# Kernel tuning notes

Measured on AMD Instinct MI355X. Metric: run time of the kernel, lower is better.

The kernel has to match this reference:

```python
import jax, jax.numpy as jnp
import numpy as np

BN_EPS = 1e-5


def setup_inputs() -> dict:
    key = jax.random.key(0)
    ks = jax.random.split(key, 12)
    B, C, S, M = 128, 512, 128, 512  # batch, model_dim, spatial_size, middle_ss
    lim_in = 1.0 / np.sqrt(S)   # torch Linear init bound, fan_in = S
    lim_mid = 1.0 / np.sqrt(M)
    return {
        "query": jax.random.normal(ks[0], (B, C, S), jnp.float32),
        "key":   jax.random.normal(ks[1], (B, C, S), jnp.float32),
        "value": jax.random.normal(ks[2], (B, C, S), jnp.float32),
        "Wq": jax.random.uniform(ks[3], (M, S), jnp.float32, -lim_in, lim_in),
        "bq": jax.random.uniform(ks[4], (M,), jnp.float32, -lim_in, lim_in),
        "Wk": jax.random.uniform(ks[5], (M, S), jnp.float32, -lim_in, lim_in),
        "bk": jax.random.uniform(ks[6], (M,), jnp.float32, -lim_in, lim_in),
        "Wv": jax.random.uniform(ks[7], (M, S), jnp.float32, -lim_in, lim_in),
        "bv": jax.random.uniform(ks[8], (M,), jnp.float32, -lim_in, lim_in),
        "Wf": jax.random.uniform(ks[9], (S, M), jnp.float32, -lim_mid, lim_mid),
        "bf": jax.random.uniform(ks[10], (S,), jnp.float32, -lim_mid, lim_mid),
        "gamma": jnp.ones((C,), jnp.float32),
        "beta": jnp.zeros((C,), jnp.float32),
    }


def reference(query, key, value, Wq, bq, Wk, bk, Wv, bv, Wf, bf, gamma, beta):
    residual = value                                  # [B, C, S]
    q = jnp.einsum('bcs,ms->bcm', query, Wq) + bq     # [B, C, M]
    k = jnp.einsum('bcs,ms->bcm', key, Wk) + bk
    v = jnp.einsum('bcs,ms->bcm', value, Wv) + bv
    scale = k.shape[-1] ** (-0.5)
    scores = jnp.einsum('bim,bjm->bij', q, k) * scale  # [B, C, C]
    attention = jax.nn.softmax(scores, axis=2)
    context = jnp.einsum('bij,bjm->bim', attention, v)  # [B, C, M]
    out = jnp.einsum('bcm,sm->bcs', context, Wf) + bf    # [B, C, S]
    # BatchNorm1d (training mode): stats over (batch, spatial) per channel
    mean = jnp.mean(out, axis=(0, 2), keepdims=True)
    var = jnp.mean(jnp.square(out - mean), axis=(0, 2), keepdims=True)
    out = (out - mean) * jax.lax.rsqrt(var + BN_EPS)
    out = out * gamma[None, :, None] + beta[None, :, None]
    out = jax.nn.relu(out)
    out = residual + out
    return (out, attention)
```

## Files before the change

kernel.cpp:

```cpp
#include <hip/hip_runtime.h>
#include <math.h>

#define B_  128
#define C_  512
#define S_  128
#define M_  512
#define BN_EPS 1e-5f

typedef __attribute__((ext_vector_type(8))) short   short8;
typedef __attribute__((ext_vector_type(4))) float   floatx4;
typedef __attribute__((ext_vector_type(4))) unsigned short ushort4v;
typedef __attribute__((ext_vector_type(8))) unsigned short ushort8v;

__device__ __forceinline__ unsigned short f2bu(float f) {
    union { float f; unsigned int u; } c; c.f = f;
    unsigned int u = c.u;
    return (unsigned short)((u + 0x7fffu + ((u >> 16) & 1u)) >> 16);
}

__global__ __launch_bounds__(256)
void f2bf4_kernel(const float* __restrict__ a0, const float* __restrict__ a1,
                  const float* __restrict__ a2, const float* __restrict__ a3,
                  unsigned short* __restrict__ out, long n8)
{
    const float* in = (blockIdx.y == 0) ? a0 : (blockIdx.y == 1) ? a1
                    : (blockIdx.y == 2) ? a2 : a3;
    unsigned short* o = out + (long)blockIdx.y * (n8 * 8);
    const long i = (long)blockIdx.x * 256 + threadIdx.x;
    if (i >= n8) return;
    const float4* p = (const float4*)in + 2 * i;
    const float4 x = p[0], y = p[1];
    ushort4v u0, u1;
    u0.x = f2bu(x.x); u0.y = f2bu(x.y); u0.z = f2bu(x.z); u0.w = f2bu(x.w);
    u1.x = f2bu(y.x); u1.y = f2bu(y.y); u1.z = f2bu(y.z); u1.w = f2bu(y.w);
    ((ushort4v*)o)[2 * i]     = u0;
    ((ushort4v*)o)[2 * i + 1] = u1;
}

__global__ __launch_bounds__(256)
void pack_bias_zero_stats(const float* __restrict__ bq, const float* __restrict__ bk,
                          const float* __restrict__ bv, float* __restrict__ bqkv,
                          float* __restrict__ stats)
{
    const int t = blockIdx.x * 256 + threadIdx.x;
    if (t < 512)            bqkv[t] = bq[t];
    else if (t < 1024)      bqkv[t] = bk[t - 512];
    else if (t < 1536)      bqkv[t] = bv[t - 1024];
    else if (t < 1536 + 2 * C_) stats[t - 1536] = 0.f;
}

__global__ __launch_bounds__(512, 4)
void proj_kernel(const float* __restrict__ qf, const float* __restrict__ kf,
                 const float* __restrict__ vf, const unsigned short* __restrict__ Wbf,
                 const float* __restrict__ bqkv, unsigned short* __restrict__ outbf)
{
    const int z = blockIdx.y;
    const float* A = (z == 0 ? qf : z == 1 ? kf : vf) + (long)blockIdx.x * 64 * S_;
    const unsigned short* W = Wbf + (long)z * M_ * S_;
    const float* bias = bqkv + z * M_;
    unsigned short* O = outbf + (long)z * ((long)B_ * C_ * M_) + (long)blockIdx.x * 64 * M_;

    __shared__ unsigned short As[64][40];
    __shared__ unsigned short Bs[512][40];

    const int t    = threadIdx.x;
    const int lane = t & 63;
    const int wave = t >> 6;
    const int lrow = lane & 15;
    const int quad = lane >> 4;
    const int cb   = wave * 64;

    floatx4 acc[4][4] = {};

    const int ar = t >> 3;
    const int ac = (t & 7) * 4;
    const int sr = t >> 2;
    const int sc = (t & 3) * 8;

    for (int k0 = 0; k0 < S_; k0 += 32) {
        const float4 av = *(const float4*)(A + (long)ar * S_ + k0 + ac);
        ushort4v au;
        au.x = f2bu(av.x); au.y = f2bu(av.y); au.z = f2bu(av.z); au.w = f2bu(av.w);
        *(ushort4v*)&As[ar][ac] = au;
        #pragma unroll
        for (int i = 0; i < 4; ++i) {
            const int r = sr + i * 128;
            *(short8*)&Bs[r][sc] = *(const short8*)(W + (long)r * S_ + k0 + sc);
        }
        __syncthreads();

        short8 af[4];
        #pragma unroll
        for (int i = 0; i < 4; ++i)
            af[i] = *(const short8*)&As[i * 16 + lrow][quad * 8];
        #pragma unroll
        for (int j = 0; j < 4; ++j) {
            const short8 bfr = *(const short8*)&Bs[cb + j * 16 + lrow][quad * 8];
            #pragma unroll
            for (int i = 0; i < 4; ++i)
                acc[i][j] = __builtin_amdgcn_mfma_f32_16x16x32_bf16(
                    af[i], bfr, acc[i][j], 0, 0, 0);
        }
        __syncthreads();
    }

    unsigned short* scr = &Bs[wave * 64][0];
    const int rr = lane >> 3;
    const int rc = (lane & 7) * 8;
    #pragma unroll
    for (int i = 0; i < 4; ++i) {
        #pragma unroll
        for (int j = 0; j < 4; ++j) {
            const float bv = bias[cb + j * 16 + lrow];
            #pragma unroll
            for (int rg = 0; rg < 4; ++rg)
                scr[(quad * 4 + rg) * 72 + j * 16 + lrow] = f2bu(acc[i][j][rg] + bv);
        }
        #pragma unroll
        for (int p = 0; p < 2; ++p) {
            const int row = p * 8 + rr;
            const ushort8v v = *(const ushort8v*)&scr[row * 72 + rc];
            *(ushort8v*)&O[(long)(i * 16 + row) * M_ + cb + rc] = v;
        }
    }
}

template<bool STATS>
__global__ __launch_bounds__(256)
void gemm_bf16(const unsigned short* __restrict__ A, const unsigned short* __restrict__ Bm,
               const float* __restrict__ bias, void* __restrict__ Cc,
               int M, int N, int K, int ldA, int ldB, int ldC,
               long sA, long sB, long sC, long sBias, float scale, int outMode,
               float* __restrict__ statsOut)
{
    const int bz = blockIdx.z;
    A  += (long)bz * sA;
    Bm += (long)bz * sB;
    if (bias) bias += (long)bz * sBias;

    __shared__ unsigned short As[128][72];
    __shared__ unsigned short Bs[128][72];

    const int t    = threadIdx.x;
    const int lane = t & 63;
    const int wave = t >> 6;
    const int wm   = (wave >> 1) * 64;
    const int wn   = (wave & 1) * 64;
    const int lrow = lane & 15;
    const int quad = lane >> 4;
    const int row0 = blockIdx.x * 128;
    const int col0 = blockIdx.y * 128;

    floatx4 acc[4][4] = {};

    const int srow = t >> 3;
    const int skc  = (t & 7) * 8;

    for (int k0 = 0; k0 < K; k0 += 64) {
        #pragma unroll
        for (int i = 0; i < 4; ++i) {
            const int r = srow + i * 32;
            *(short8*)&As[r][skc] =
                *(const short8*)(A + (long)(row0 + r) * ldA + k0 + skc);
            *(short8*)&Bs[r][skc] =
                *(const short8*)(Bm + (long)(col0 + r) * ldB + k0 + skc);
        }
        __syncthreads();

        #pragma unroll
        for (int kb = 0; kb < 2; ++kb) {
            short8 af[4], bfr[4];
            #pragma unroll
            for (int i = 0; i < 4; ++i)
                af[i]  = *(const short8*)&As[wm + i * 16 + lrow][kb * 32 + quad * 8];
            #pragma unroll
            for (int j = 0; j < 4; ++j)
                bfr[j] = *(const short8*)&Bs[wn + j * 16 + lrow][kb * 32 + quad * 8];
            #pragma unroll
            for (int i = 0; i < 4; ++i)
                #pragma unroll
                for (int j = 0; j < 4; ++j)
                    acc[i][j] = __builtin_amdgcn_mfma_f32_16x16x32_bf16(
                        af[i], bfr[j], acc[i][j], 0, 0, 0);
        }
        __syncthreads();
    }

    float rs[4][4], rss[4][4];
    if (STATS) {
        #pragma unroll
        for (int i = 0; i < 4; ++i)
            #pragma unroll
            for (int rg = 0; rg < 4; ++rg) { rs[i][rg] = 0.f; rss[i][rg] = 0.f; }
    }
    #pragma unroll
    for (int j = 0; j < 4; ++j) {
        const int col = col0 + wn + j * 16 + lrow;
        const float bv = bias ? bias[col] : 0.0f;
        #pragma unroll
        for (int i = 0; i < 4; ++i) {
            const int rbase = row0 + wm + i * 16 + quad * 4;
            #pragma unroll
            for (int reg = 0; reg < 4; ++reg) {
                const float val = acc[i][j][reg] * scale + bv;
                const int r = rbase + reg;
                if (STATS) { rs[i][reg] += val; rss[i][reg] += val * val; }
                if (outMode == 0) {
                    ((float*)Cc)[(long)bz * sC + (long)r * ldC + col] = val;
                } else if (outMode == 1) {
                    ((unsigned short*)Cc)[(long)bz * sC + (long)r * ldC + col] = f2bu(val);
                } else {
                    ((unsigned short*)Cc)[((long)(r >> 9)) * 65536 + (long)col * 512 + (r & 511)] = f2bu(val);
                }
            }
        }
    }
    if (STATS) {
        #pragma unroll
        for (int i = 0; i < 4; ++i) {
            #pragma unroll
            for (int reg = 0; reg < 4; ++reg) {
                float s = rs[i][reg], ss = rss[i][reg];
                #pragma unroll
                for (int off = 1; off < 16; off <<= 1) {
                    s  += __shfl_xor(s,  off);
                    ss += __shfl_xor(ss, off);
                }
                if (lrow == 0) {
                    const int r = row0 + wm + i * 16 + quad * 4 + reg;
                    atomicAdd(&statsOut[r],      s);
                    atomicAdd(&statsOut[C_ + r], ss);
                }
            }
        }
    }
}

__global__ __launch_bounds__(512, 4)
void scores_softmax_kernel(const unsigned short* __restrict__ q_bf,
                           const unsigned short* __restrict__ k_bf,
                           float* __restrict__ attn,
                           unsigned short* __restrict__ attnbf,
                           float scale)
{
    const int bid = blockIdx.x;
    const int b   = (bid & 7) * 16 + ((bid >> 3) >> 3);
    const int r0  = ((bid >> 3) & 7) * 64;

    const unsigned short* qg = q_bf + (long)b * C_ * M_;
    const unsigned short* kg = k_bf + (long)b * C_ * M_;
    float* ab           = attn   + (long)b * C_ * C_;
    unsigned short* abf = attnbf + (long)b * C_ * C_;

    __shared__ unsigned short qs[64][40];
    __shared__ unsigned short ks[512][40];
    __shared__ float red[64][9];

    const int t    = threadIdx.x;
    const int lane = t & 63;
    const int wave = t >> 6;
    const int lrow = lane & 15;
    const int quad = lane >> 4;
    const int cb   = wave * 64;

    floatx4 acc[4][4] = {};

    const int sr = t >> 2;
    const int sc = (t & 3) * 8;

    for (int k0 = 0; k0 < M_; k0 += 32) {
        if (t < 256)
            *(short8*)&qs[t >> 2][sc] =
                *(const short8*)(qg + (long)(r0 + (t >> 2)) * M_ + k0 + sc);
        #pragma unroll
        for (int i = 0; i < 4; ++i) {
            const int r = sr + i * 128;
            *(short8*)&ks[r][sc] = *(const short8*)(kg + (long)r * M_ + k0 + sc);
        }
        __syncthreads();

        short8 af[4];
        #pragma unroll
        for (int i = 0; i < 4; ++i)
            af[i] = *(const short8*)&qs[i * 16 + lrow][quad * 8];
        #pragma unroll
        for (int j = 0; j < 4; ++j) {
            const short8 bfr = *(const short8*)&ks[cb + j * 16 + lrow][quad * 8];
            #pragma unroll
            for (int i = 0; i < 4; ++i)
                acc[i][j] = __builtin_amdgcn_mfma_f32_16x16x32_bf16(
                    af[i], bfr, acc[i][j], 0, 0, 0);
        }
        __syncthreads();
    }

    float mx[4][4];
    #pragma unroll
    for (int i = 0; i < 4; ++i) {
        #pragma unroll
        for (int rg = 0; rg < 4; ++rg) {
            float m = fmaxf(fmaxf(acc[i][0][rg], acc[i][1][rg]),
                            fmaxf(acc[i][2][rg], acc[i][3][rg]));
            #pragma unroll
            for (int off = 1; off < 16; off <<= 1) m = fmaxf(m, __shfl_xor(m, off));
            mx[i][rg] = m;
        }
    }
    if (lrow == 0) {
        #pragma unroll
        for (int i = 0; i < 4; ++i)
            #pragma unroll
            for (int rg = 0; rg < 4; ++rg)
                red[i * 16 + quad * 4 + rg][wave] = mx[i][rg];
    }
    __syncthreads();
    #pragma unroll
    for (int i = 0; i < 4; ++i) {
        #pragma unroll
        for (int rg = 0; rg < 4; ++rg) {
            const int row = i * 16 + quad * 4 + rg;
            float m = red[row][0];
            #pragma unroll
            for (int w = 1; w < 8; ++w) m = fmaxf(m, red[row][w]);
            mx[i][rg] = m;
        }
    }
    __syncthreads();

    float sm[4][4];
    #pragma unroll
    for (int i = 0; i < 4; ++i) {
        #pragma unroll
        for (int rg = 0; rg < 4; ++rg) {
            float s = 0.f;
            #pragma unroll
            for (int j = 0; j < 4; ++j) {
                const float e = __expf((acc[i][j][rg] - mx[i][rg]) * scale);
                acc[i][j][rg] = e;
                s += e;
            }
            #pragma unroll
            for (int off = 1; off < 16; off <<= 1) s += __shfl_xor(s, off);
            sm[i][rg] = s;
        }
    }
    if (lrow == 0) {
        #pragma unroll
        for (int i = 0; i < 4; ++i)
            #pragma unroll
            for (int rg = 0; rg < 4; ++rg)
                red[i * 16 + quad * 4 + rg][wave] = sm[i][rg];
    }
    __syncthreads();
    #pragma unroll
    for (int i = 0; i < 4; ++i) {
        #pragma unroll
        for (int rg = 0; rg < 4; ++rg) {
            const int row = i * 16 + quad * 4 + rg;
            float s = red[row][0];
            #pragma unroll
            for (int w = 1; w < 8; ++w) s += red[row][w];
            sm[i][rg] = 1.0f / s;
        }
    }
    __syncthreads();

    float* scr = (float*)&ks[wave * 64][0];
    const int rr = lane >> 3;
    const int rc = (lane & 7) * 4;
    #pragma unroll
    for (int i = 0; i < 4; ++i) {
        #pragma unroll
        for (int j = 0; j < 4; ++j)
            #pragma unroll
            for (int rg = 0; rg < 4; ++rg)
                scr[(quad * 4 + rg) * 68 + j * 16 + lrow] = acc[i][j][rg] * sm[i][rg];
        #pragma unroll
        for (int pr = 0; pr < 2; ++pr) {
            #pragma unroll
            for (int pc = 0; pc < 2; ++pc) {
                const int row = pr * 8 + rr;
                const int col = pc * 32 + rc;
                const float4 v = *(const float4*)&scr[row * 68 + col];
                const long gr = r0 + i * 16 + row;
                const long gc = cb + col;
                *(float4*)&ab[gr * C_ + gc] = v;
                ushort4v u;
                u.x = f2bu(v.x); u.y = f2bu(v.y); u.z = f2bu(v.z); u.w = f2bu(v.w);
                *(ushort4v*)&abf[gr * C_ + gc] = u;
            }
        }
    }
}

__global__ __launch_bounds__(256)
void bn_apply_kernel(const float* __restrict__ outp, const float* __restrict__ value,
                     const float* __restrict__ stats, const float* __restrict__ gamma,
                     const float* __restrict__ beta, float* __restrict__ out)
{
    const long i4 = (long)blockIdx.x * 256 + threadIdx.x;
    const int  c  = (int)((i4 >> 5) & (C_ - 1));

    const float invn = 1.0f / (float)(B_ * S_);
    const float mean = stats[c] * invn;
    const float var  = stats[C_ + c] * invn - mean * mean;
    const float istd = rsqrtf(var + BN_EPS);
    const float g    = gamma[c] * istd;
    const float bc   = beta[c] - mean * g;

    const float4 x = ((const float4*)outp)[i4];
    const float4 r = ((const float4*)value)[i4];
    float4 y;
    y.x = fmaxf(fmaf(x.x, g, bc), 0.f) + r.x;
    y.y = fmaxf(fmaf(x.y, g, bc), 0.f) + r.y;
    y.z = fmaxf(fmaf(x.z, g, bc), 0.f) + r.z;
    y.w = fmaxf(fmaf(x.w, g, bc), 0.f) + r.w;
    ((float4*)out)[i4] = y;
}

extern "C" void kernel_launch(void* const* d_in, const int* in_sizes, int n_in,
                              void* d_out, int out_size, void* d_ws, size_t ws_size,
                              hipStream_t stream)
{
    const float* query = (const float*)d_in[0];
    const float* key   = (const float*)d_in[1];
    const float* value = (const float*)d_in[2];
    const float* Wq    = (const float*)d_in[3];
    const float* bq    = (const float*)d_in[4];
    const float* Wk    = (const float*)d_in[5];
    const float* bk    = (const float*)d_in[6];
    const float* Wv    = (const float*)d_in[7];
    const float* bv    = (const float*)d_in[8];
    const float* Wf    = (const float*)d_in[9];
    const float* bf    = (const float*)d_in[10];
    const float* gamma = (const float*)d_in[11];
    const float* beta  = (const float*)d_in[12];

    const long BC  = (long)B_ * C_;
    const long BCM = BC * M_;
    const long BCS = BC * S_;
    const long BCC = BC * C_;

    unsigned short* w      = (unsigned short*)d_ws;
    unsigned short* q_bf   = w;
    unsigned short* k_bf   = q_bf + BCM;
    unsigned short* v2_bf  = k_bf + BCM;
    unsigned short* attnbf = v2_bf + BCM;
    unsigned short* vwT    = attnbf + BCC;
    unsigned short* Wq_bf  = vwT + (long)B_ * S_ * C_;
    unsigned short* Wf_bf  = Wq_bf + 3L * M_ * S_;
    float* outp  = (float*)(Wf_bf + (long)S_ * M_);
    float* stats = outp + BCS;
    float* bqkv = (float*)attnbf;

    float* out0 = (float*)d_out;
    float* attn = out0 + BCS;

    const float scale = 1.0f / sqrtf((float)M_);
    dim3 blk(256);
    dim3 blk512(512);

    f2bf4_kernel<<<dim3(32, 4), blk, 0, stream>>>(Wq, Wk, Wv, Wf, Wq_bf,
                                                  (long)M_ * S_ / 8);
    pack_bias_zero_stats<<<dim3(10), blk, 0, stream>>>(bq, bk, bv, bqkv, stats);

    proj_kernel<<<dim3(1024, 3), blk512, 0, stream>>>(
        query, key, value, Wq_bf, bqkv, q_bf);

    scores_softmax_kernel<<<dim3(1024), blk512, 0, stream>>>(
        q_bf, k_bf, attn, attnbf, scale);

    gemm_bf16<false><<<dim3(512, 1, 1), blk, 0, stream>>>(
        v2_bf, Wf_bf, bf, vwT, (int)BC, S_, M_, M_, M_, 0,
        0, 0, 0, 0, 1.0f, 2, nullptr);

    gemm_bf16<true><<<dim3(4, 1, 128), blk, 0, stream>>>(
        attnbf, vwT, nullptr, outp, C_, S_, C_, C_, C_, S_,
        (long)C_ * C_, (long)S_ * C_, (long)C_ * S_, 0, 1.0f, 0, stats);

    bn_apply_kernel<<<dim3(BCS / 4 / 256), blk, 0, stream>>>(
        outp, value, stats, gamma, beta, out0);
}
```

Baseline: 523.8 us.

## Make projection kernel persistent with resident weight quarter and double-buffered A tiles

The QKV projection kernel now launches a small persistent grid. Each block loads a 128-column quarter of the bf16 weight matrix into shared memory once, then loops over row tiles of the input. The next fp32 input tile is prefetched into registers and stored to a second shared buffer while the current tile is processed. This removes the repeated weight reloads of the old per-tile kernel and overlaps input loads with MFMA work. The cost is that each input row is now read four times, once per column quarter, and shared-memory use per block is higher.

```diff
diff --git a/kernel.cpp b/kernel.cpp
--- a/kernel.cpp
+++ b/kernel.cpp
@@ -49,79 +49,125 @@
     else if (t < 1536 + 2 * C_) stats[t - 1536] = 0.f;
 }
 
+__device__ __forceinline__ void cvt16(const float4* p, ushort8v& lo, ushort8v& hi) {
+    lo[0] = f2bu(p[0].x); lo[1] = f2bu(p[0].y); lo[2] = f2bu(p[0].z); lo[3] = f2bu(p[0].w);
+    lo[4] = f2bu(p[1].x); lo[5] = f2bu(p[1].y); lo[6] = f2bu(p[1].z); lo[7] = f2bu(p[1].w);
+    hi[0] = f2bu(p[2].x); hi[1] = f2bu(p[2].y); hi[2] = f2bu(p[2].z); hi[3] = f2bu(p[2].w);
+    hi[4] = f2bu(p[3].x); hi[5] = f2bu(p[3].y); hi[6] = f2bu(p[3].z); hi[7] = f2bu(p[3].w);
+}
+
 __global__ __launch_bounds__(512, 4)
 void proj_kernel(const float* __restrict__ qf, const float* __restrict__ kf,
                  const float* __restrict__ vf, const unsigned short* __restrict__ Wbf,
                  const float* __restrict__ bqkv, unsigned short* __restrict__ outbf)
 {
-    const int z = blockIdx.y;
-    const float* A = (z == 0 ? qf : z == 1 ? kf : vf) + (long)blockIdx.x * 64 * S_;
-    const unsigned short* W = Wbf + (long)z * M_ * S_;
-    const float* bias = bqkv + z * M_;
-    unsigned short* O = outbf + (long)z * ((long)B_ * C_ * M_) + (long)blockIdx.x * 64 * M_;
-
-    __shared__ unsigned short As[64][40];
-    __shared__ unsigned short Bs[512][40];
+    const int zq = blockIdx.y;
+    const int z  = zq >> 2;
+    const int q  = zq & 3;
+    const float* Ag = (z == 0 ? qf : z == 1 ? kf : vf);
+    const unsigned short* W = Wbf + (long)z * M_ * S_ + (long)q * 128 * S_;
+    unsigned short* O = outbf + (long)z * ((long)B_ * C_) * M_ + q * 128;
+
+    __shared__ unsigned short Ws[4][128][40];
+    __shared__ unsigned short As[2][4][64][40];
 
     const int t    = threadIdx.x;
     const int lane = t & 63;
     const int wave = t >> 6;
+    const int wr   = wave >> 2;
+    const int wc   = wave & 3;
     const int lrow = lane & 15;
     const int quad = lane >> 4;
-    const int cb   = wave * 64;
-
-    floatx4 acc[4][4] = {};
+
+    {
+        const int r  = t >> 2;
+        const int ko = (t & 3) * 8;
+        #pragma unroll
+        for (int c = 0; c < 4; ++c)
+            *(short8*)&Ws[c][r][ko] = *(const short8*)(W + (long)r * S_ + c * 32 + ko);
+    }
+
+    float bcol[2];
+    #pragma unroll
+    for (int j = 0; j < 2; ++j)
+        bcol[j] = bqkv[z * M_ + q * 128 + wc * 32 + j * 16 + lrow];
 
     const int ar = t >> 3;
-    const int ac = (t & 7) * 4;
-    const int sr = t >> 2;
-    const int sc = (t & 3) * 8;
-
-    for (int k0 = 0; k0 < S_; k0 += 32) {
-        const float4 av = *(const float4*)(A + (long)ar * S_ + k0 + ac);
-        ushort4v au;
-        au.x = f2bu(av.x); au.y = f2bu(av.y); au.z = f2bu(av.z); au.w = f2bu(av.w);
-        *(ushort4v*)&As[ar][ac] = au;
-        #pragma unroll
-        for (int i = 0; i < 4; ++i) {
-            const int r = sr + i * 128;
-            *(short8*)&Bs[r][sc] = *(const short8*)(W + (long)r * S_ + k0 + sc);
-        }
-        __syncthreads();
-
-        short8 af[4];
-        #pragma unroll
-        for (int i = 0; i < 4; ++i)
-            af[i] = *(const short8*)&As[i * 16 + lrow][quad * 8];
-        #pragma unroll
-        for (int j = 0; j < 4; ++j) {
-            const short8 bfr = *(const short8*)&Bs[cb + j * 16 + lrow][quad * 8];
-            #pragma unroll
-            for (int i = 0; i < 4; ++i)
-                acc[i][j] = __builtin_amdgcn_mfma_f32_16x16x32_bf16(
-                    af[i], bfr, acc[i][j], 0, 0, 0);
-        }
-        __syncthreads();
-    }
-
-    unsigned short* scr = &Bs[wave * 64][0];
-    const int rr = lane >> 3;
-    const int rc = (lane & 7) * 8;
-    #pragma unroll
-    for (int i = 0; i < 4; ++i) {
-        #pragma unroll
-        for (int j = 0; j < 4; ++j) {
-            const float bv = bias[cb + j * 16 + lrow];
-            #pragma unroll
-            for (int rg = 0; rg < 4; ++rg)
-                scr[(quad * 4 + rg) * 72 + j * 16 + lrow] = f2bu(acc[i][j][rg] + bv);
-        }
-        #pragma unroll
-        for (int p = 0; p < 2; ++p) {
-            const int row = p * 8 + rr;
-            const ushort8v v = *(const ushort8v*)&scr[row * 72 + rc];
-            *(ushort8v*)&O[(long)(i * 16 + row) * M_ + cb + rc] = v;
-        }
+    const int ac = (t & 7) * 16;
+
+    float4 pre[4];
+    int s = blockIdx.x;
+
+    {
+        const float* Ap = Ag + ((long)s * 64 + ar) * S_ + ac;
+        #pragma unroll
+        for (int i = 0; i < 4; ++i) pre[i] = ((const float4*)Ap)[i];
+        ushort8v lo, hi;
+        cvt16(pre, lo, hi);
+        *(ushort8v*)&As[0][ac >> 5][ar][ac & 31]       = lo;
+        *(ushort8v*)&As[0][ac >> 5][ar][(ac & 31) + 8] = hi;
+    }
+
+    int cur = 0;
+    while (s < 1024) {
+        const int snext   = s + 43;
+        const bool hasNext = (snext < 1024);
+        __syncthreads();
+
+        if (hasNext) {
+            const float* Ap = Ag + ((long)snext * 64 + ar) * S_ + ac;
+            #pragma unroll
+            for (int i = 0; i < 4; ++i) pre[i] = ((const float4*)Ap)[i];
+        }
+
+        floatx4 acc[2][2] = {};
+        #pragma unroll
+        for (int c = 0; c < 4; ++c) {
+            short8 af[2], bfr[2];
+            #pragma unroll
+            for (int i = 0; i < 2; ++i)
+                af[i]  = *(const short8*)&As[cur][c][wr * 32 + i * 16 + lrow][quad * 8];
+            #pragma unroll
+            for (int j = 0; j < 2; ++j)
+                bfr[j] = *(const short8*)&Ws[c][wc * 32 + j * 16 + lrow][quad * 8];
+            #pragma unroll
+            for (int i = 0; i < 2; ++i)
+                #pragma unroll
+                for (int j = 0; j < 2; ++j)
+                    acc[i][j] = __builtin_amdgcn_mfma_f32_16x16x32_bf16(
+                        af[i], bfr[j], acc[i][j], 0, 0, 0);
+        }
+        __syncthreads();
+
+        unsigned short* scr = &As[cur][0][0][0];
+        #pragma unroll
+        for (int i = 0; i < 2; ++i)
+            #pragma unroll
+            for (int j = 0; j < 2; ++j)
+                #pragma unroll
+                for (int rg = 0; rg < 4; ++rg)
+                    scr[(wr * 32 + i * 16 + quad * 4 + rg) * 136 + wc * 32 + j * 16 + lrow] =
+                        f2bu(acc[i][j][rg] + bcol[j]);
+
+        if (hasNext) {
+            ushort8v lo, hi;
+            cvt16(pre, lo, hi);
+            *(ushort8v*)&As[cur ^ 1][ac >> 5][ar][ac & 31]       = lo;
+            *(ushort8v*)&As[cur ^ 1][ac >> 5][ar][(ac & 31) + 8] = hi;
+        }
+        __syncthreads();
+
+        {
+            const int row = t >> 3;
+            const int c16 = (t & 7) * 16;
+            const ushort8v v0 = *(const ushort8v*)&scr[row * 136 + c16];
+            const ushort8v v1 = *(const ushort8v*)&scr[row * 136 + c16 + 8];
+            unsigned short* op = &O[((long)s * 64 + row) * M_ + c16];
+            *(ushort8v*)op       = v0;
+            *(ushort8v*)(op + 8) = v1;
+        }
+        cur ^= 1;
+        s = snext;
     }
 }
 
@@ -464,7 +510,7 @@
                                                   (long)M_ * S_ / 8);
     pack_bias_zero_stats<<<dim3(10), blk, 0, stream>>>(bq, bk, bv, bqkv, stats);
 
-    proj_kernel<<<dim3(1024, 3), blk512, 0, stream>>>(
+    proj_kernel<<<dim3(43, 12), blk512, 0, stream>>>(
         query, key, value, Wq_bf, bqkv, q_bf);
 
     scores_softmax_kernel<<<dim3(1024), blk512, 0, stream>>>(
```

Measured after the change: 533.2 us. No clear change (+1.8%).

## Load GEMM fragments directly from global memory, dropping LDS staging and barriers

Applied to the files above, without the earlier changes.

The projection and scores kernels now load MFMA A/B fragments straight from global memory into registers instead of staging tiles through shared memory with two barriers per k-step. The projection epilogue writes bf16 results directly with scattered 2-byte stores rather than staging them through LDS for coalesced vector stores. The scores kernel gets a dedicated per-wave scratch buffer, and launch bounds drop to 2 blocks per SM to leave more registers. This removes LDS traffic and synchronisation, but the direct loads are less coalesced, each wave re-reads the shared tiles through cache, and the uncoalesced epilogue stores may be costly.

```diff
diff --git a/kernel.cpp b/kernel.cpp
--- a/kernel.cpp
+++ b/kernel.cpp
@@ -49,79 +49,58 @@
     else if (t < 1536 + 2 * C_) stats[t - 1536] = 0.f;
 }
 
-__global__ __launch_bounds__(512, 4)
+__global__ __launch_bounds__(512, 2)
 void proj_kernel(const float* __restrict__ qf, const float* __restrict__ kf,
                  const float* __restrict__ vf, const unsigned short* __restrict__ Wbf,
                  const float* __restrict__ bqkv, unsigned short* __restrict__ outbf)
 {
-    const int z = blockIdx.y;
-    const float* A = (z == 0 ? qf : z == 1 ? kf : vf) + (long)blockIdx.x * 64 * S_;
+    const int z     = blockIdx.y;
+    const int strip = blockIdx.x;
+    const float* A = (z == 0 ? qf : z == 1 ? kf : vf) + (long)strip * 64 * S_;
     const unsigned short* W = Wbf + (long)z * M_ * S_;
-    const float* bias = bqkv + z * M_;
-    unsigned short* O = outbf + (long)z * ((long)B_ * C_ * M_) + (long)blockIdx.x * 64 * M_;
-
-    __shared__ unsigned short As[64][40];
-    __shared__ unsigned short Bs[512][40];
-
-    const int t    = threadIdx.x;
-    const int lane = t & 63;
-    const int wave = t >> 6;
+    unsigned short* O = outbf + (long)z * ((long)B_ * C_ * M_) + (long)strip * 64 * M_;
+
+    const int lane = threadIdx.x & 63;
+    const int wave = threadIdx.x >> 6;
     const int lrow = lane & 15;
     const int quad = lane >> 4;
     const int cb   = wave * 64;
 
     floatx4 acc[4][4] = {};
 
-    const int ar = t >> 3;
-    const int ac = (t & 7) * 4;
-    const int sr = t >> 2;
-    const int sc = (t & 3) * 8;
-
-    for (int k0 = 0; k0 < S_; k0 += 32) {
-        const float4 av = *(const float4*)(A + (long)ar * S_ + k0 + ac);
-        ushort4v au;
-        au.x = f2bu(av.x); au.y = f2bu(av.y); au.z = f2bu(av.z); au.w = f2bu(av.w);
-        *(ushort4v*)&As[ar][ac] = au;
+    #pragma unroll
+    for (int c = 0; c < 4; ++c) {
+        short8 af[4], bfr[4];
         #pragma unroll
         for (int i = 0; i < 4; ++i) {
-            const int r = sr + i * 128;
-            *(short8*)&Bs[r][sc] = *(const short8*)(W + (long)r * S_ + k0 + sc);
-        }
-        __syncthreads();
-
-        short8 af[4];
-        #pragma unroll
-        for (int i = 0; i < 4; ++i)
-            af[i] = *(const short8*)&As[i * 16 + lrow][quad * 8];
-        #pragma unroll
-        for (int j = 0; j < 4; ++j) {
-            const short8 bfr = *(const short8*)&Bs[cb + j * 16 + lrow][quad * 8];
-            #pragma unroll
-            for (int i = 0; i < 4; ++i)
+            const float* ap = A + (long)(i * 16 + lrow) * S_ + c * 32 + quad * 8;
+            const float4 a0 = *(const float4*)ap;
+            const float4 a1 = *(const float4*)(ap + 4);
+            short8 v;
+            v[0] = f2bu(a0.x); v[1] = f2bu(a0.y); v[2] = f2bu(a0.z); v[3] = f2bu(a0.w);
+            v[4] = f2bu(a1.x); v[5] = f2bu(a1.y); v[6] = f2bu(a1.z); v[7] = f2bu(a1.w);
+            af[i] = v;
+        }
+        #pragma unroll
+        for (int j = 0; j < 4; ++j)
+            bfr[j] = *(const short8*)(W + (long)(cb + j * 16 + lrow) * S_ + c * 32 + quad * 8);
+        #pragma unroll
+        for (int i = 0; i < 4; ++i)
+            #pragma unroll
+            for (int j = 0; j < 4; ++j)
                 acc[i][j] = __builtin_amdgcn_mfma_f32_16x16x32_bf16(
-                    af[i], bfr, acc[i][j], 0, 0, 0);
-        }
-        __syncthreads();
-    }
-
-    unsigned short* scr = &Bs[wave * 64][0];
-    const int rr = lane >> 3;
-    const int rc = (lane & 7) * 8;
-    #pragma unroll
-    for (int i = 0; i < 4; ++i) {
-        #pragma unroll
-        for (int j = 0; j < 4; ++j) {
-            const float bv = bias[cb + j * 16 + lrow];
+                    af[i], bfr[j], acc[i][j], 0, 0, 0);
+    }
+
+    #pragma unroll
+    for (int j = 0; j < 4; ++j) {
+        const int col = cb + j * 16 + lrow;
+        const float bv = bqkv[z * M_ + col];
+        #pragma unroll
+        for (int i = 0; i < 4; ++i)
             #pragma unroll
             for (int rg = 0; rg < 4; ++rg)
-                scr[(quad * 4 + rg) * 72 + j * 16 + lrow] = f2bu(acc[i][j][rg] + bv);
-        }
-        #pragma unroll
-        for (int p = 0; p < 2; ++p) {
-            const int row = p * 8 + rr;
-            const ushort8v v = *(const ushort8v*)&scr[row * 72 + rc];
-            *(ushort8v*)&O[(long)(i * 16 + row) * M_ + cb + rc] = v;
-        }
+                O[(long)(i * 16 + quad * 4 + rg) * M_ + col] = f2bu(acc[i][j][rg] + bv);
     }
 }
 
@@ -236,7 +215,7 @@
     }
 }
 
-__global__ __launch_bounds__(512, 4)
+__global__ __launch_bounds__(512, 2)
 void scores_softmax_kernel(const unsigned short* __restrict__ q_bf,
                            const unsigned short* __restrict__ k_bf,
                            float* __restrict__ attn,
@@ -244,7 +223,7 @@
                            float scale)
 {
     const int bid = blockIdx.x;
-    const int b   = (bid & 7) * 16 + ((bid >> 3) >> 3);
+    const int b   = (bid & 7) * 16 + (bid >> 6);
     const int r0  = ((bid >> 3) & 7) * 64;
 
     const unsigned short* qg = q_bf + (long)b * C_ * M_;
@@ -252,9 +231,8 @@
     float* ab           = attn   + (long)b * C_ * C_;
     unsigned short* abf = attnbf + (long)b * C_ * C_;
 
-    __shared__ unsigned short qs[64][40];
-    __shared__ unsigned short ks[512][40];
     __shared__ float red[64][9];
+    __shared__ float scr[8][16][68];
 
     const int t    = threadIdx.x;
     const int lane = t & 63;
@@ -265,33 +243,24 @@
 
     floatx4 acc[4][4] = {};
 
-    const int sr = t >> 2;
-    const int sc = (t & 3) * 8;
-
+    const unsigned short* qbase = qg + (long)(r0 + lrow) * M_ + quad * 8;
+    const unsigned short* kbase = kg + (long)(cb + lrow) * M_ + quad * 8;
+
+    #pragma unroll 2
     for (int k0 = 0; k0 < M_; k0 += 32) {
-        if (t < 256)
-            *(short8*)&qs[t >> 2][sc] =
-                *(const short8*)(qg + (long)(r0 + (t >> 2)) * M_ + k0 + sc);
-        #pragma unroll
-        for (int i = 0; i < 4; ++i) {
-            const int r = sr + i * 128;
-            *(short8*)&ks[r][sc] = *(const short8*)(kg + (long)r * M_ + k0 + sc);
-        }
-        __syncthreads();
-
-        short8 af[4];
-        #pragma unroll
-        for (int i = 0; i < 4; ++i)
-            af[i] = *(const short8*)&qs[i * 16 + lrow][quad * 8];
-        #pragma unroll
-        for (int j = 0; j < 4; ++j) {
-            const short8 bfr = *(const short8*)&ks[cb + j * 16 + lrow][quad * 8];
-            #pragma unroll
-            for (int i = 0; i < 4; ++i)
+        short8 af[4], bfr[4];
+        #pragma unroll
+        for (int i = 0; i < 4; ++i)
+            af[i]  = *(const short8*)(qbase + (long)i * 16 * M_ + k0);
+        #pragma unroll
+        for (int j = 0; j < 4; ++j)
+            bfr[j] = *(const short8*)(kbase + (long)j * 16 * M_ + k0);
+        #pragma unroll
+        for (int i = 0; i < 4; ++i)
+            #pragma unroll
+            for (int j = 0; j < 4; ++j)
                 acc[i][j] = __builtin_amdgcn_mfma_f32_16x16x32_bf16(
-                    af[i], bfr, acc[i][j], 0, 0, 0);
-        }
-        __syncthreads();
+                    af[i], bfr[j], acc[i][j], 0, 0, 0);
     }
 
     float mx[4][4];
@@ -363,9 +332,8 @@
             sm[i][rg] = 1.0f / s;
         }
     }
-    __syncthreads();
-
-    float* scr = (float*)&ks[wave * 64][0];
+
+    float* sw = &scr[wave][0][0];
     const int rr = lane >> 3;
     const int rc = (lane & 7) * 4;
     #pragma unroll
@@ -374,14 +342,14 @@
         for (int j = 0; j < 4; ++j)
             #pragma unroll
             for (int rg = 0; rg < 4; ++rg)
-                scr[(quad * 4 + rg) * 68 + j * 16 + lrow] = acc[i][j][rg] * sm[i][rg];
+                sw[(quad * 4 + rg) * 68 + j * 16 + lrow] = acc[i][j][rg] * sm[i][rg];
         #pragma unroll
         for (int pr = 0; pr < 2; ++pr) {
             #pragma unroll
             for (int pc = 0; pc < 2; ++pc) {
                 const int row = pr * 8 + rr;
                 const int col = pc * 32 + rc;
-                const float4 v = *(const float4*)&scr[row * 68 + col];
+                const float4 v = *(const float4*)&sw[row * 68 + col];
                 const long gr = r0 + i * 16 + row;
                 const long gc = cb + col;
                 *(float4*)&ab[gr * C_ + gc] = v;
```

New measurement: 660.5 us. +26.1%, slower.
